# Kernel tuning notes

Measured on AMD Instinct MI355X. Metric: run time of the kernel, lower is better.

The kernel has to match this reference:

```python
import jax, jax.numpy as jnp
import numpy as np

N_NODES = 100000
N_EDGES = 1600000
RBF_DIM = 64
DIM = 64


def shifted_softplus(x):
    # torch.nn.Softplus(beta=0.5, threshold=14): (1/0.5)*log(1+exp(0.5*x)),
    # with linear passthrough when 0.5*x > 14.
    half = 0.5 * x
    return jnp.where(half > 14.0, x, 2.0 * jnp.logaddexp(0.0, half))


def setup_inputs() -> dict:
    key = jax.random.key(0)
    ks = jax.random.split(key, 8)
    node_weight = jax.random.normal(ks[0], (N_NODES, DIM), dtype=jnp.float32)
    rbf_out = jax.random.normal(ks[1], (N_EDGES, RBF_DIM), dtype=jnp.float32)
    # Linear params (torch Linear: y = x @ W.T + b); store W already transposed as (in,out)
    s1 = 1.0 / np.sqrt(RBF_DIM)
    s2 = 1.0 / np.sqrt(DIM)
    W1 = jax.random.uniform(ks[2], (RBF_DIM, DIM), jnp.float32, -s1, s1)
    b1 = jax.random.uniform(ks[3], (DIM,), jnp.float32, -s1, s1)
    W2 = jax.random.uniform(ks[4], (DIM, DIM), jnp.float32, -s2, s2)
    b2 = jax.random.uniform(ks[5], (DIM,), jnp.float32, -s2, s2)
    src = jax.random.randint(ks[6], (N_EDGES,), 0, N_NODES, dtype=jnp.int32)
    dst = jax.random.randint(ks[7], (N_EDGES,), 0, N_NODES, dtype=jnp.int32)
    return {
        "node_weight": node_weight, "rbf_out": rbf_out,
        "W1": W1, "b1": b1, "W2": W2, "b2": b2,
        "src": src, "dst": dst, "n_nodes": N_NODES,
    }


def reference(node_weight, rbf_out, W1, b1, W2, b2, src, dst, n_nodes):
    # edge MLP: Linear -> shifted softplus -> Linear, on rbf features  [E, dim]
    e = shifted_softplus(rbf_out @ W1 + b1) @ W2 + b2
    # gather source node weight per edge, multiply by edge filter      [E, dim]
    m = node_weight[src] * e
    # scatter-sum messages into destination nodes                      [N, dim]
    h = jax.ops.segment_sum(m, dst, num_segments=n_nodes)
    return h
```

## Files before the change

kernel.cpp:

```cpp
#include <hip/hip_runtime.h>
#include <math.h>

typedef short bf16x8 __attribute__((ext_vector_type(8)));
typedef float f32x4 __attribute__((ext_vector_type(4)));

__device__ __forceinline__ short f2bf(float f) {
    union { float f; unsigned u; } v; v.f = f;
    unsigned r = v.u + 0x7fffu + ((v.u >> 16) & 1u);
    return (short)(r >> 16);
}

__device__ __forceinline__ float ssp(float x) {
    float h = 0.5f * x;
    return 2.0f * (fmaxf(h, 0.0f) + __logf(1.0f + __expf(-fabsf(h))));
}

__global__ __launch_bounds__(256, 2) void cfconv_kernel(
    const float* __restrict__ nw, const float* __restrict__ rbf,
    const float* __restrict__ W1, const float* __restrict__ b1,
    const float* __restrict__ W2, const float* __restrict__ b2,
    const int* __restrict__ src, const int* __restrict__ dst,
    float* __restrict__ out, int n_edges)
{
    __shared__ __align__(16) short lds_h[4][16 * 72];

    const int tid  = threadIdx.x;
    const int wave = tid >> 6;
    const int lane = tid & 63;
    const int l16  = lane & 15;
    const int quad = lane >> 4;

    bf16x8 w1f[2][4], w2f[2][4];
    #pragma unroll
    for (int ks = 0; ks < 2; ++ks) {
        #pragma unroll
        for (int nt = 0; nt < 4; ++nt) {
            const int col = l16 + 16 * nt;
            const int k0  = quad * 8 + 32 * ks;
            bf16x8 a, b;
            #pragma unroll
            for (int j = 0; j < 8; ++j) {
                a[j] = f2bf(W1[(k0 + j) * 64 + col]);
                b[j] = f2bf(W2[(k0 + j) * 64 + col]);
            }
            w1f[ks][nt] = a;
            w2f[ks][nt] = b;
        }
    }
    float b1v[4], b2v[4];
    #pragma unroll
    for (int nt = 0; nt < 4; ++nt) {
        b1v[nt] = b1[l16 + 16 * nt];
        b2v[nt] = b2[l16 + 16 * nt];
    }

    short* myh = lds_h[wave];
    const int ntiles = (n_edges + 15) >> 4;
    const int gw = blockIdx.x * 4 + wave;
    const int stride = gridDim.x * 4;

    for (int t = gw; t < ntiles; t += stride) {
        const int e0 = t * 16;

        int arow = e0 + l16;
        if (arow >= n_edges) arow = n_edges - 1;
        const float* rp = rbf + (size_t)arow * 64 + quad * 8;
        bf16x8 af[2];
        #pragma unroll
        for (int ks = 0; ks < 2; ++ks) {
            float4 lo = *(const float4*)(rp + 32 * ks);
            float4 hi = *(const float4*)(rp + 32 * ks + 4);
            bf16x8 a;
            a[0] = f2bf(lo.x); a[1] = f2bf(lo.y); a[2] = f2bf(lo.z); a[3] = f2bf(lo.w);
            a[4] = f2bf(hi.x); a[5] = f2bf(hi.y); a[6] = f2bf(hi.z); a[7] = f2bf(hi.w);
            af[ks] = a;
        }

        f32x4 acc[4] = { {0.f,0.f,0.f,0.f}, {0.f,0.f,0.f,0.f},
                         {0.f,0.f,0.f,0.f}, {0.f,0.f,0.f,0.f} };
        #pragma unroll
        for (int nt = 0; nt < 4; ++nt)
            #pragma unroll
            for (int ks = 0; ks < 2; ++ks)
                acc[nt] = __builtin_amdgcn_mfma_f32_16x16x32_bf16(
                    af[ks], w1f[ks][nt], acc[nt], 0, 0, 0);

        #pragma unroll
        for (int nt = 0; nt < 4; ++nt)
            #pragma unroll
            for (int r = 0; r < 4; ++r)
                myh[(quad * 4 + r) * 72 + l16 + 16 * nt] =
                    f2bf(ssp(acc[nt][r] + b1v[nt]));

        bf16x8 hf[2];
        #pragma unroll
        for (int ks = 0; ks < 2; ++ks)
            hf[ks] = *(const bf16x8*)(myh + l16 * 72 + quad * 8 + 32 * ks);

        f32x4 acc2[4] = { {0.f,0.f,0.f,0.f}, {0.f,0.f,0.f,0.f},
                          {0.f,0.f,0.f,0.f}, {0.f,0.f,0.f,0.f} };
        #pragma unroll
        for (int nt = 0; nt < 4; ++nt)
            #pragma unroll
            for (int ks = 0; ks < 2; ++ks)
                acc2[nt] = __builtin_amdgcn_mfma_f32_16x16x32_bf16(
                    hf[ks], w2f[ks][nt], acc2[nt], 0, 0, 0);

        #pragma unroll
        for (int r = 0; r < 4; ++r) {
            const int e = e0 + quad * 4 + r;
            if (e < n_edges) {
                const int s = src[e], d = dst[e];
                const float* nwp = nw + (size_t)s * 64;
                float* op = out + (size_t)d * 64;
                #pragma unroll
                for (int nt = 0; nt < 4; ++nt) {
                    const int col = l16 + 16 * nt;
                    atomicAdd(op + col, (acc2[nt][r] + b2v[nt]) * nwp[col]);
                }
            }
        }
    }
}

extern "C" void kernel_launch(void* const* d_in, const int* in_sizes, int n_in,
                              void* d_out, int out_size, void* d_ws, size_t ws_size,
                              hipStream_t stream) {
    const float* nw  = (const float*)d_in[0];
    const float* rbf = (const float*)d_in[1];
    const float* W1  = (const float*)d_in[2];
    const float* b1  = (const float*)d_in[3];
    const float* W2  = (const float*)d_in[4];
    const float* b2  = (const float*)d_in[5];
    const int*   src = (const int*)d_in[6];
    const int*   dst = (const int*)d_in[7];
    float* out = (float*)d_out;
    const int n_edges = in_sizes[6];

    hipMemsetAsync(out, 0, (size_t)out_size * sizeof(float), stream);

    const int blocks = 1024;
    hipLaunchKernelGGL(cfconv_kernel, dim3(blocks), dim3(256), 0, stream,
                       nw, rbf, W1, b1, W2, b2, src, dst, out, n_edges);
}
```

Baseline: 818.6 us.

## Counting-sort edges by destination and merge same-destination atomics per lane

Adds a counting sort of edges by destination: a histogram, a block-wise scan and a permutation kernel build a dst-sorted permutation. The fused MLP kernel then walks edges in that order, with each wave taking a contiguous range of tiles. Each lane adds together runs of consecutive rows that share a destination before issuing one atomicAdd, which cuts atomic traffic and improves locality of the output writes. In exchange it adds several small preprocessing launches with their own atomics, and the rbf, src and dst reads become indirect gathers through the permutation.

```diff
diff --git a/kernel.cpp b/kernel.cpp
--- a/kernel.cpp
+++ b/kernel.cpp
@@ -14,13 +14,69 @@
     float h = 0.5f * x;
     return 2.0f * (fmaxf(h, 0.0f) + __logf(1.0f + __expf(-fabsf(h))));
 }
+
+
+__global__ void hist_kernel(const int* __restrict__ dst, int n, int* __restrict__ cnt) {
+    int i = blockIdx.x * 256 + threadIdx.x;
+    if (i < n) atomicAdd(&cnt[dst[i]], 1);
+}
+
+__global__ void blocksum_kernel(const int* __restrict__ cnt, int n, int* __restrict__ partials) {
+    __shared__ int red[256];
+    int t = threadIdx.x, base = blockIdx.x * 1024 + t * 4, s = 0;
+    #pragma unroll
+    for (int j = 0; j < 4; ++j) { int i = base + j; if (i < n) s += cnt[i]; }
+    red[t] = s; __syncthreads();
+    for (int off = 128; off > 0; off >>= 1) {
+        if (t < off) red[t] += red[t + off];
+        __syncthreads();
+    }
+    if (t == 0) partials[blockIdx.x] = red[0];
+}
+
+__global__ void scanpart_kernel(int* __restrict__ partials, int nb) {
+    __shared__ int buf[256];
+    int t = threadIdx.x;
+    if (t < nb) buf[t] = partials[t];
+    __syncthreads();
+    if (t == 0) { int run = 0; for (int i = 0; i < nb; ++i) { int v = buf[i]; buf[i] = run; run += v; } }
+    __syncthreads();
+    if (t < nb) partials[t] = buf[t];
+}
+
+__global__ void scanwrite_kernel(const int* __restrict__ cnt, int n,
+                                 const int* __restrict__ partials, int* __restrict__ cursor) {
+    __shared__ int sc[256];
+    int t = threadIdx.x, b = blockIdx.x, base = b * 1024 + t * 4;
+    int v[4], s = 0;
+    #pragma unroll
+    for (int j = 0; j < 4; ++j) { int i = base + j; v[j] = (i < n) ? cnt[i] : 0; s += v[j]; }
+    sc[t] = s; __syncthreads();
+    for (int off = 1; off < 256; off <<= 1) {
+        int y = (t >= off) ? sc[t - off] : 0;
+        __syncthreads();
+        sc[t] += y;
+        __syncthreads();
+    }
+    int run = partials[b] + sc[t] - s;
+    #pragma unroll
+    for (int j = 0; j < 4; ++j) { int i = base + j; if (i < n) cursor[i] = run; run += v[j]; }
+}
+
+__global__ void perm_kernel(const int* __restrict__ dst, int n,
+                            int* __restrict__ cursor, int* __restrict__ perm) {
+    int i = blockIdx.x * 256 + threadIdx.x;
+    if (i < n) { int p = atomicAdd(&cursor[dst[i]], 1); perm[p] = i; }
+}
+
 
 __global__ __launch_bounds__(256, 2) void cfconv_kernel(
     const float* __restrict__ nw, const float* __restrict__ rbf,
     const float* __restrict__ W1, const float* __restrict__ b1,
     const float* __restrict__ W2, const float* __restrict__ b2,
     const int* __restrict__ src, const int* __restrict__ dst,
-    float* __restrict__ out, int n_edges)
+    const int* __restrict__ perm, float* __restrict__ out,
+    int n_edges, int ntiles, int tiles_per_wave)
 {
     __shared__ __align__(16) short lds_h[4][16 * 72];
 
@@ -55,16 +111,15 @@
     }
 
     short* myh = lds_h[wave];
-    const int ntiles = (n_edges + 15) >> 4;
-    const int gw = blockIdx.x * 4 + wave;
-    const int stride = gridDim.x * 4;
-
-    for (int t = gw; t < ntiles; t += stride) {
+    const int wid = blockIdx.x * 4 + wave;
+    const int t0 = wid * tiles_per_wave;
+    const int t1 = min(t0 + tiles_per_wave, ntiles);
+
+    for (int t = t0; t < t1; ++t) {
         const int e0 = t * 16;
 
-        int arow = e0 + l16;
-        if (arow >= n_edges) arow = n_edges - 1;
-        const float* rp = rbf + (size_t)arow * 64 + quad * 8;
+        const int er = perm[min(e0 + l16, n_edges - 1)];
+        const float* rp = rbf + (size_t)er * 64 + quad * 8;
         bf16x8 af[2];
         #pragma unroll
         for (int ks = 0; ks < 2; ++ks) {
@@ -76,8 +131,7 @@
             af[ks] = a;
         }
 
-        f32x4 acc[4] = { {0.f,0.f,0.f,0.f}, {0.f,0.f,0.f,0.f},
-                         {0.f,0.f,0.f,0.f}, {0.f,0.f,0.f,0.f} };
+        f32x4 acc[4] = { {0,0,0,0}, {0,0,0,0}, {0,0,0,0}, {0,0,0,0} };
         #pragma unroll
         for (int nt = 0; nt < 4; ++nt)
             #pragma unroll
@@ -97,8 +151,7 @@
         for (int ks = 0; ks < 2; ++ks)
             hf[ks] = *(const bf16x8*)(myh + l16 * 72 + quad * 8 + 32 * ks);
 
-        f32x4 acc2[4] = { {0.f,0.f,0.f,0.f}, {0.f,0.f,0.f,0.f},
-                          {0.f,0.f,0.f,0.f}, {0.f,0.f,0.f,0.f} };
+        f32x4 acc2[4] = { {0,0,0,0}, {0,0,0,0}, {0,0,0,0}, {0,0,0,0} };
         #pragma unroll
         for (int nt = 0; nt < 4; ++nt)
             #pragma unroll
@@ -106,19 +159,31 @@
                 acc2[nt] = __builtin_amdgcn_mfma_f32_16x16x32_bf16(
                     hf[ks], w2f[ks][nt], acc2[nt], 0, 0, 0);
 
+        int dd[4], ssrc[4];
         #pragma unroll
         for (int r = 0; r < 4; ++r) {
-            const int e = e0 + quad * 4 + r;
-            if (e < n_edges) {
-                const int s = src[e], d = dst[e];
-                const float* nwp = nw + (size_t)s * 64;
-                float* op = out + (size_t)d * 64;
-                #pragma unroll
-                for (int nt = 0; nt < 4; ++nt) {
-                    const int col = l16 + 16 * nt;
-                    atomicAdd(op + col, (acc2[nt][r] + b2v[nt]) * nwp[col]);
+            const int pe = perm[min(e0 + quad * 4 + r, n_edges - 1)];
+            dd[r] = dst[pe];
+            ssrc[r] = src[pe];
+        }
+        #pragma unroll
+        for (int nt = 0; nt < 4; ++nt) {
+            const int col = l16 + 16 * nt;
+            float val[4];
+            #pragma unroll
+            for (int r = 0; r < 4; ++r)
+                val[r] = (acc2[nt][r] + b2v[nt]) * nw[(size_t)ssrc[r] * 64 + col];
+            float run = val[0];
+            int dprev = dd[0];
+            #pragma unroll
+            for (int r = 1; r < 4; ++r) {
+                if (dd[r] == dprev) run += val[r];
+                else {
+                    atomicAdd(out + (size_t)dprev * 64 + col, run);
+                    dprev = dd[r]; run = val[r];
                 }
             }
+            atomicAdd(out + (size_t)dprev * 64 + col, run);
         }
     }
 }
@@ -136,10 +201,32 @@
     const int*   dst = (const int*)d_in[7];
     float* out = (float*)d_out;
     const int n_edges = in_sizes[6];
+    const int n_nodes = in_sizes[0] / 64;
+
+    char* ws = (char*)d_ws;
+    int* cnt      = (int*)(ws);
+    int* cursor   = (int*)(ws + (size_t)n_nodes * 4);
+    int* partials = (int*)(ws + (size_t)n_nodes * 8);
+    int* perm     = (int*)(ws + (size_t)n_nodes * 8 + 1024);
 
     hipMemsetAsync(out, 0, (size_t)out_size * sizeof(float), stream);
-
+    hipMemsetAsync(cnt, 0, (size_t)n_nodes * 4, stream);
+
+    const int nb = (n_nodes + 1023) / 1024;
+    hipLaunchKernelGGL(hist_kernel, dim3((n_edges + 255) / 256), dim3(256), 0, stream,
+                       dst, n_edges, cnt);
+    hipLaunchKernelGGL(blocksum_kernel, dim3(nb), dim3(256), 0, stream,
+                       cnt, n_nodes, partials);
+    hipLaunchKernelGGL(scanpart_kernel, dim3(1), dim3(256), 0, stream, partials, nb);
+    hipLaunchKernelGGL(scanwrite_kernel, dim3(nb), dim3(256), 0, stream,
+                       cnt, n_nodes, partials, cursor);
+    hipLaunchKernelGGL(perm_kernel, dim3((n_edges + 255) / 256), dim3(256), 0, stream,
+                       dst, n_edges, cursor, perm);
+
+    const int ntiles = (n_edges + 15) / 16;
     const int blocks = 1024;
+    const int tpw = (ntiles + blocks * 4 - 1) / (blocks * 4);
     hipLaunchKernelGGL(cfconv_kernel, dim3(blocks), dim3(256), 0, stream,
-                       nw, rbf, W1, b1, W2, b2, src, dst, out, n_edges);
-}
+                       nw, rbf, W1, b1, W2, b2, src, dst, perm, out,
+                       n_edges, ntiles, tpw);
+}
```

New measurement: 968.5 us. 1.18x slower.
